# Kernel tuning notes

Measured on AMD Instinct MI355X. Metric: run time of the kernel, lower is better.

Reference implementation:

```python
import jax, jax.numpy as jnp
import numpy as np

B, N, C = 4, 8192, 512
H = 4
D = C // H  # 128
HID = 4 * C  # mlp hidden, mlp_ratio=4.0
SCALE = D ** -0.5
EPS = 1e-5


def layernorm(x, w, b):
    mu = jnp.mean(x, axis=-1, keepdims=True)
    var = jnp.var(x, axis=-1, keepdims=True)
    return (x - mu) * jax.lax.rsqrt(var + EPS) * w + b


def setup_inputs() -> dict:
    key = jax.random.key(0)
    ks = jax.random.split(key, 8)
    s = lambda fan_in: 1.0 / np.sqrt(fan_in)
    return {
        "x": jax.random.normal(ks[0], (B, N, C), jnp.float32),
        "norm1_w": jnp.ones((C,), jnp.float32),
        "norm1_b": jnp.zeros((C,), jnp.float32),
        "qkv_w": jax.random.normal(ks[1], (C, 3 * C), jnp.float32) * s(C),
        "qkv_b": jnp.zeros((3 * C,), jnp.float32),
        "lnk_w": jnp.ones((D,), jnp.float32),
        "lnk_b": jnp.zeros((D,), jnp.float32),
        "lnv_w": jnp.ones((D,), jnp.float32),
        "lnv_b": jnp.zeros((D,), jnp.float32),
        "proj_w": jax.random.normal(ks[2], (C, C), jnp.float32) * s(C),
        "proj_b": jnp.zeros((C,), jnp.float32),
        "norm2_w": jnp.ones((C,), jnp.float32),
        "norm2_b": jnp.zeros((C,), jnp.float32),
        "mlp_w1": jax.random.normal(ks[3], (C, HID), jnp.float32) * s(C),
        "mlp_b1": jnp.zeros((HID,), jnp.float32),
        "mlp_w2": jax.random.normal(ks[4], (HID, C), jnp.float32) * s(HID),
        "mlp_b2": jnp.zeros((C,), jnp.float32),
    }


def reference(x, norm1_w, norm1_b, qkv_w, qkv_b, lnk_w, lnk_b, lnv_w, lnv_b,
              proj_w, proj_b, norm2_w, norm2_b, mlp_w1, mlp_b1, mlp_w2, mlp_b2):
    shortcut = x
    xn = layernorm(x, norm1_w, norm1_b)
    qkv = xn @ qkv_w + qkv_b                       # [B,N,3C]
    qkv = qkv.reshape(B, N, 3, H, D).transpose(2, 0, 3, 1, 4)  # [3,B,H,N,D]
    q, k, v = qkv[0], qkv[1], qkv[2]
    k = layernorm(k, lnk_w, lnk_b)
    v = layernorm(v, lnv_w, lnv_b)
    context = jnp.einsum('bhnd,bhne->bhde', k, v)   # [B,H,D,D] small context
    attn = jnp.einsum('bhnd,bhde->bhne', q, context) * SCALE  # [B,H,N,D]
    attn = attn.transpose(0, 2, 1, 3).reshape(B, N, C)
    x1 = shortcut + (attn @ proj_w + proj_b)
    h = layernorm(x1, norm2_w, norm2_b)
    mlp = jax.nn.gelu(h @ mlp_w1 + mlp_b1, approximate=False) @ mlp_w2 + mlp_b2
    return x1 + mlp
```

## Files before the change

### kernel.cpp

```cpp
#include <hip/hip_runtime.h>
#include <stdint.h>


#define B_    4
#define N_    8192
#define C_    512
#define H_    4
#define D_    128
#define HID_  2048
#define M_    (B_*N_)
#define EPS_  1e-5f
#define SCALE_ 0.08838834764831845f

typedef unsigned short u16;
typedef __attribute__((ext_vector_type(8))) __bf16 bfrag_t;
typedef __attribute__((ext_vector_type(4))) float  f4_t;

__device__ __forceinline__ float bf2f(u16 a) {
    unsigned int u = ((unsigned int)a) << 16; float f;
    __builtin_memcpy(&f, &u, 4); return f;
}
__device__ __forceinline__ u16 f2bf(float f) {
    unsigned int u; __builtin_memcpy(&u, &f, 4);
    u += 0x7FFFu + ((u >> 16) & 1u);
    return (u16)(u >> 16);
}
__device__ __forceinline__ u16 f2bf_fast(float f) {
    unsigned int u; __builtin_memcpy(&u, &f, 4);
    return (u16)((u + 0x8000u) >> 16);
}

__device__ __forceinline__ float fast_gelu(float x) {
    const float kA = 2.3022084f;
    const float kB = 0.1029435f;
    float x2 = x * x;
    float e1 = __builtin_amdgcn_exp2f(x * (kB * x2 + kA));
    return x - x * __builtin_amdgcn_rcpf(e1 + 1.0f);
}

__device__ __forceinline__ void gld16(u16* lds, const u16* g) {
    void* gp = const_cast<u16*>(g);
    __builtin_amdgcn_global_load_lds((__attribute__((address_space(1))) void*)gp,
                                     (__attribute__((address_space(3))) void*)lds,
                                     16, 0, 0);
}

__global__ void wtrans(const float* __restrict__ in, u16* __restrict__ out,
                       int K, int Ncols) {
    long idx = (long)blockIdx.x * 256 + threadIdx.x;
    long total = (long)K * Ncols;
    if (idx >= total) return;
    int k = (int)(idx % K), n = (int)(idx / K);
    out[idx] = f2bf(in[(long)k * Ncols + n]);
}

__global__ __launch_bounds__(256)
void ln_rows(const float* __restrict__ in, const float* __restrict__ w,
             const float* __restrict__ b, u16* __restrict__ out) {
    long row = blockIdx.x;
    int t = threadIdx.x;
    const float* p = in + row * 512;
    float v0 = p[t], v1 = p[t + 256];
    float s = v0 + v1, q = v0 * v0 + v1 * v1;
    #pragma unroll
    for (int o = 32; o >= 1; o >>= 1) { s += __shfl_xor(s, o, 64); q += __shfl_xor(q, o, 64); }
    __shared__ float sh[8];
    int wv = t >> 6, l = t & 63;
    if (l == 0) { sh[wv] = s; sh[4 + wv] = q; }
    __syncthreads();
    s = sh[0] + sh[1] + sh[2] + sh[3];
    q = sh[4] + sh[5] + sh[6] + sh[7];
    float mu = s * (1.f / 512.f);
    float var = q * (1.f / 512.f) - mu * mu;
    float rs = rsqrtf(var + EPS_);
    out[row * 512 + t]       = f2bf((v0 - mu) * rs * w[t] + b[t]);
    out[row * 512 + t + 256] = f2bf((v1 - mu) * rs * w[t + 256] + b[t + 256]);
}

__global__ __launch_bounds__(256)
void lnkv(const u16* __restrict__ qkv,
          const float* __restrict__ kw, const float* __restrict__ kb,
          const float* __restrict__ vw, const float* __restrict__ vb,
          u16* __restrict__ kT, u16* __restrict__ vT) {
    int bh = blockIdx.x;
    int b = bh >> 2, h = bh & 3;
    int n0 = blockIdx.y * 64;
    int wv = threadIdx.x >> 6, l = threadIdx.x & 63;
    __shared__ u16 lk[128 * 68], lv[128 * 68];

    for (int r = wv; r < 64; r += 4) {
        long base = ((long)b * N_ + n0 + r) * 1536 + h * 128;
        {
            float x0 = bf2f(qkv[base + 512 + l]), x1 = bf2f(qkv[base + 512 + 64 + l]);
            float s = x0 + x1, q = x0 * x0 + x1 * x1;
            #pragma unroll
            for (int o = 32; o >= 1; o >>= 1) { s += __shfl_xor(s, o, 64); q += __shfl_xor(q, o, 64); }
            float mu = s * (1.f / 128.f), var = q * (1.f / 128.f) - mu * mu;
            float rs = rsqrtf(var + EPS_);
            lk[l * 68 + r]        = f2bf((x0 - mu) * rs * kw[l] + kb[l]);
            lk[(l + 64) * 68 + r] = f2bf((x1 - mu) * rs * kw[l + 64] + kb[l + 64]);
        }
        {
            float x0 = bf2f(qkv[base + 1024 + l]), x1 = bf2f(qkv[base + 1024 + 64 + l]);
            float s = x0 + x1, q = x0 * x0 + x1 * x1;
            #pragma unroll
            for (int o = 32; o >= 1; o >>= 1) { s += __shfl_xor(s, o, 64); q += __shfl_xor(q, o, 64); }
            float mu = s * (1.f / 128.f), var = q * (1.f / 128.f) - mu * mu;
            float rs = rsqrtf(var + EPS_);
            lv[l * 68 + r]        = f2bf((x0 - mu) * rs * vw[l] + vb[l]);
            lv[(l + 64) * 68 + r] = f2bf((x1 - mu) * rs * vw[l + 64] + vb[l + 64]);
        }
    }
    __syncthreads();
    long obase = (long)bh * D_ * N_;
    #pragma unroll 4
    for (int i = 0; i < 32; i++) {
        int idx = i * 256 + threadIdx.x;
        int d = idx >> 6, nn = idx & 63;
        kT[obase + (long)d * N_ + n0 + nn] = lk[d * 68 + nn];
        vT[obase + (long)d * N_ + n0 + nn] = lv[d * 68 + nn];
    }
}

__global__ void ctxfin(const float* __restrict__ ctxP, u16* __restrict__ ctxN) {
    int idx = blockIdx.x * 256 + threadIdx.x;
    if (idx >= 16 * 16384) return;
    int bh = idx >> 14, r = idx & 16383;
    const float* p = ctxP + (long)bh * 262144 + r;
    float s = 0.f;
    #pragma unroll
    for (int q = 0; q < 16; q++) s += p[q * 16384];
    ctxN[idx] = f2bf(s * SCALE_);
}

template<int MODE, int KTOT, int ZDIV>
__global__ __launch_bounds__(256)
void gemm_bt(const u16* __restrict__ A, int lda, int64_t aZ1, int64_t aZ2,
             const u16* __restrict__ Bt, int ldb, int64_t bZ1, int64_t bZ2,
             void* __restrict__ outv, int ldo, int64_t oZ1, int64_t oZ2,
             const float* __restrict__ bias, const float* __restrict__ resid, int ldr) {
    __shared__ __align__(16) u16 sA[128 * 32];
    __shared__ __align__(16) u16 sB[128 * 32];
    const int z = blockIdx.z;
    const int z1 = z / ZDIV, z2 = z % ZDIV;
    A  += z1 * aZ1 + z2 * aZ2;
    Bt += z1 * bZ1 + z2 * bZ2;
    const int64_t ooff = z1 * oZ1 + z2 * oZ2;
    const int m0 = blockIdx.x * 128, n0 = blockIdx.y * 128;
    const int tid = threadIdx.x, wave = tid >> 6, lane = tid & 63;
    const int wr = wave >> 1, wc = wave & 1;

    f4_t acc[4][4];
    #pragma unroll
    for (int i = 0; i < 4; i++)
        #pragma unroll
        for (int j = 0; j < 4; j++) acc[i][j] = (f4_t){0.f, 0.f, 0.f, 0.f};

    const int c0 = wave * 64 + lane, c1 = 256 + wave * 64 + lane;
    const int r0 = c0 >> 2, e0 = (c0 & 3) * 8;
    const int r1 = c1 >> 2, e1 = (c1 & 3) * 8;
    const u16* a0 = A + (int64_t)(m0 + r0) * lda + e0;
    const u16* a1 = A + (int64_t)(m0 + r1) * lda + e1;
    const u16* b0 = Bt + (int64_t)(n0 + r0) * ldb + e0;
    const u16* b1 = Bt + (int64_t)(n0 + r1) * ldb + e1;
    u16* lA0 = &sA[wave * 512];        u16* lA1 = &sA[2048 + wave * 512];
    u16* lB0 = &sB[wave * 512];        u16* lB1 = &sB[2048 + wave * 512];

    const int qd = lane >> 4, md = lane & 15;
    int aoff[4], boff[4];
    #pragma unroll
    for (int i = 0; i < 4; i++) {
        aoff[i] = (wr * 64 + i * 16 + md) * 32 + qd * 8;
        boff[i] = (wc * 64 + i * 16 + md) * 32 + qd * 8;
    }

    #pragma unroll 4
    for (int kt = 0; kt < KTOT; kt += 32) {
        __syncthreads();
        gld16(lA0, a0 + kt);  gld16(lA1, a1 + kt);
        gld16(lB0, b0 + kt);  gld16(lB1, b1 + kt);
        __syncthreads();
        bfrag_t af[4], bf[4];
        #pragma unroll
        for (int i = 0; i < 4; i++) af[i] = *(const bfrag_t*)&sA[aoff[i]];
        #pragma unroll
        for (int i = 0; i < 4; i++) bf[i] = *(const bfrag_t*)&sB[boff[i]];
        #pragma unroll
        for (int mi = 0; mi < 4; mi++)
            #pragma unroll
            for (int ni = 0; ni < 4; ni++)
                acc[mi][ni] = __builtin_amdgcn_mfma_f32_16x16x32_bf16(
                    af[mi], bf[ni], acc[mi][ni], 0, 0, 0);
    }

    #pragma unroll
    for (int mi = 0; mi < 4; mi++) {
        #pragma unroll
        for (int r = 0; r < 4; r++) {
            int m = m0 + wr * 64 + mi * 16 + qd * 4 + r;
            int64_t rowo = ooff + (int64_t)m * ldo;
            #pragma unroll
            for (int ni = 0; ni < 4; ni++) {
                int n = n0 + wc * 64 + ni * 16 + md;
                float v = acc[mi][ni][r];
                if (MODE == 0)
                    ((u16*)outv)[rowo + n] = f2bf_fast(v);
                else
                    ((float*)outv)[rowo + n] = v;
            }
        }
    }
}

#define LD_(p)      (*(const bfrag_t*)(p))
#define FENCE_      asm volatile("" ::: "memory")
#define BAR_        do { FENCE_; __builtin_amdgcn_s_barrier(); FENCE_; } while (0)
#define WVM4_       asm volatile("s_waitcnt vmcnt(4)" ::: "memory")
#define WVM0_       asm volatile("s_waitcnt vmcnt(0)" ::: "memory")
#define MFMA_(va, vb, c) c = __builtin_amdgcn_mfma_f32_16x16x32_bf16(va, vb, c, 0, 0, 0)
#define MM16_(I0) do { __builtin_amdgcn_s_setprio(1); \
  MFMA_(a0,b0,acc[(I0)+0][0]); MFMA_(a0,b1,acc[(I0)+0][1]); MFMA_(a0,b2,acc[(I0)+0][2]); MFMA_(a0,b3,acc[(I0)+0][3]); \
  MFMA_(a1,b0,acc[(I0)+1][0]); MFMA_(a1,b1,acc[(I0)+1][1]); MFMA_(a1,b2,acc[(I0)+1][2]); MFMA_(a1,b3,acc[(I0)+1][3]); \
  MFMA_(a2,b0,acc[(I0)+2][0]); MFMA_(a2,b1,acc[(I0)+2][1]); MFMA_(a2,b2,acc[(I0)+2][2]); MFMA_(a2,b3,acc[(I0)+2][3]); \
  MFMA_(a3,b0,acc[(I0)+3][0]); MFMA_(a3,b1,acc[(I0)+3][1]); MFMA_(a3,b2,acc[(I0)+3][2]); MFMA_(a3,b3,acc[(I0)+3][3]); \
  __builtin_amdgcn_s_setprio(0); } while (0)
#define STGA_(nb, kk, tt) do { \
  u16* d_ = lds + (nb) * 32768 + (kk) * 8192 + wid * 512; \
  const u16* s_ = aS + (int64_t)(tt) * 64 + (kk) * 32; \
  gld16(d_, s_); gld16(d_ + 4096, s_ + a128); } while (0)
#define STGB_(nb, kk, tt) do { \
  u16* d_ = lds + (nb) * 32768 + 16384 + (kk) * 8192 + wid * 512; \
  const u16* s_ = bS + (int64_t)(tt) * 64 + (kk) * 32; \
  gld16(d_, s_); gld16(d_ + 4096, s_ + b128); } while (0)

template<int MODE, int KTOT>
__global__ __launch_bounds__(512, 2)
void gemm256(const u16* __restrict__ A, int lda, int64_t aZ,
             const u16* __restrict__ Bt, int ldb, int64_t bZ,
             void* __restrict__ outv, int ldo, int64_t oZ,
             const float* __restrict__ bias, const float* __restrict__ resid, int ldr) {
    __shared__ __align__(16) u16 lds[65536];
    const int z = blockIdx.z;
    A += (int64_t)z * aZ;
    Bt += (int64_t)z * bZ;
    const int64_t ooff = (int64_t)z * oZ;
    const int gx = gridDim.x, gy = gridDim.y;
    const int lid = blockIdx.x + blockIdx.y * gx;
    int bx, by;
    if ((gx & 7) == 0) {
        const int j = lid >> 3;
        bx = (gx >> 3) * (lid & 7) + j / gy;
        by = j % gy;
    } else { bx = blockIdx.x; by = blockIdx.y; }
    const int m0 = bx * 256, n0 = by * 256;
    const int tid = threadIdx.x, wid = tid >> 6, lane = tid & 63;
    const int wr = wid >> 2, wc = wid & 3;
    const int md = lane & 15, qd = lane >> 4;

    f4_t acc[8][4];
    #pragma unroll
    for (int i = 0; i < 8; ++i)
        #pragma unroll
        for (int j = 0; j < 4; ++j) acc[i][j] = (f4_t){0.f, 0.f, 0.f, 0.f};

    const int srow = tid >> 2;
    const int scol = ((tid & 3) ^ ((tid >> 3) & 3)) * 8;
    const u16* aS = A  + (int64_t)(m0 + srow) * lda + scol;
    const u16* bS = Bt + (int64_t)(n0 + srow) * ldb + scol;
    const int64_t a128 = (int64_t)lda * 128, b128 = (int64_t)ldb * 128;

    const int xq = (qd ^ ((md >> 1) & 3)) * 16;
    const int aRow = (wr * 128 + md) * 64;
    const int bRow = (wc * 64 + md) * 64;
    const char* ldsc = (const char*)lds;

    constexpr int NT = KTOT / 64;

    {
        STGA_(0, 0, 0); STGB_(0, 0, 0); STGA_(0, 1, 0); STGB_(0, 1, 0);
        WVM4_; BAR_;
    }

    #pragma unroll 2
    for (int t = 0; t < NT; ++t) {
        const int cur = t & 1, nb = cur ^ 1;
        const char* cA = ldsc + cur * 65536 + aRow;
        const char* cB = ldsc + cur * 65536 + 32768 + bRow;
        const bool st = (t + 1 < NT);
        bfrag_t a0, a1, a2, a3, b0, b1, b2, b3;

        a0 = LD_(cA + xq);        a1 = LD_(cA + 1024 + xq);
        a2 = LD_(cA + 2048 + xq); a3 = LD_(cA + 3072 + xq);
        b0 = LD_(cB + xq);        b1 = LD_(cB + 1024 + xq);
        b2 = LD_(cB + 2048 + xq); b3 = LD_(cB + 3072 + xq);
        if (st) STGA_(nb, 0, t + 1);
        BAR_;
        MM16_(0);

        a0 = LD_(cA + 4096 + xq); a1 = LD_(cA + 5120 + xq);
        a2 = LD_(cA + 6144 + xq); a3 = LD_(cA + 7168 + xq);
        if (st) STGB_(nb, 0, t + 1);
        BAR_;
        MM16_(4);

        if (st) { WVM4_; } else { WVM0_; }
        BAR_;

        a0 = LD_(cA + 16384 + xq);        a1 = LD_(cA + 17408 + xq);
        a2 = LD_(cA + 18432 + xq);        a3 = LD_(cA + 19456 + xq);
        b0 = LD_(cB + 16384 + xq);        b1 = LD_(cB + 17408 + xq);
        b2 = LD_(cB + 18432 + xq);        b3 = LD_(cB + 19456 + xq);
        if (st) STGA_(nb, 1, t + 1);
        BAR_;
        MM16_(0);

        a0 = LD_(cA + 20480 + xq); a1 = LD_(cA + 21504 + xq);
        a2 = LD_(cA + 22528 + xq); a3 = LD_(cA + 23552 + xq);
        if (st) STGB_(nb, 1, t + 1);
        BAR_;
        MM16_(4);

        if (st) { WVM4_; } else { WVM0_; }
        BAR_;
    }

    #pragma unroll
    for (int i = 0; i < 8; ++i) {
        #pragma unroll
        for (int rr = 0; rr < 4; ++rr) {
            const int m = m0 + wr * 128 + i * 16 + qd * 4 + rr;
            const int64_t rowo = ooff + (int64_t)m * ldo;
            #pragma unroll
            for (int j = 0; j < 4; ++j) {
                const int n = n0 + wc * 64 + j * 16 + md;
                float v = acc[i][j][rr];
                if (MODE == 1 || MODE == 2 || MODE == 3) v += bias[n];
                if (MODE == 2) v = fast_gelu(v);
                if (MODE == 3) v += resid[ooff + (int64_t)m * ldr + n];
                if (MODE == 3)
                    ((float*)outv)[rowo + n] = v;
                else
                    ((u16*)outv)[rowo + n] = f2bf_fast(v);
            }
        }
    }
}

#undef LD_
#undef FENCE_
#undef BAR_
#undef WVM4_
#undef WVM0_
#undef MFMA_
#undef MM16_
#undef STGA_
#undef STGB_

extern "C" void kernel_launch(void* const* d_in, const int* in_sizes, int n_in,
                              void* d_out, int out_size, void* d_ws, size_t ws_size,
                              hipStream_t stream) {
    const float* x      = (const float*)d_in[0];
    const float* n1w    = (const float*)d_in[1];
    const float* n1b    = (const float*)d_in[2];
    const float* qkv_w  = (const float*)d_in[3];
    const float* qkv_b  = (const float*)d_in[4];
    const float* lnk_w  = (const float*)d_in[5];
    const float* lnk_b  = (const float*)d_in[6];
    const float* lnv_w  = (const float*)d_in[7];
    const float* lnv_b  = (const float*)d_in[8];
    const float* proj_w = (const float*)d_in[9];
    const float* proj_b = (const float*)d_in[10];
    const float* n2w    = (const float*)d_in[11];
    const float* n2b    = (const float*)d_in[12];
    const float* w1     = (const float*)d_in[13];
    const float* b1     = (const float*)d_in[14];
    const float* w2     = (const float*)d_in[15];
    const float* b2     = (const float*)d_in[16];
    float* out = (float*)d_out;

    char* ws = (char*)d_ws;
    u16*  qkvWT = (u16*)(ws + 0);
    u16*  projT = (u16*)(ws + 1572864);
    u16*  w1T   = (u16*)(ws + 2097152);
    u16*  w2T   = (u16*)(ws + 4194304);
    u16*  ctxN  = (u16*)(ws + 7340032);
    u16*  bufA  = (u16*)(ws + 7864320);
    u16*  qkv   = (u16*)(ws + 41418752);
    u16*  hid   = (u16*)(ws + 41418752);
    u16*  kT    = (u16*)(ws + 142082048);
    u16*  vT    = (u16*)(ws + 175636480);
    float* ctxP = (float*)(ws + 7864320);
    u16*  wqT   = (u16*)(ws + 7864320 + 16777216);

    dim3 blk(256);
    dim3 blk5(512);

    wtrans<<<dim3(512 * 1536 / 256), blk, 0, stream>>>(qkv_w, qkvWT, 512, 1536);
    wtrans<<<dim3(512 * 512 / 256),  blk, 0, stream>>>(proj_w, projT, 512, 512);
    wtrans<<<dim3(512 * 2048 / 256), blk, 0, stream>>>(w1, w1T, 512, 2048);
    wtrans<<<dim3(2048 * 512 / 256), blk, 0, stream>>>(w2, w2T, 2048, 512);

    ln_rows<<<dim3(M_), blk, 0, stream>>>(x, n1w, n1b, bufA);

    gemm256<1, 512><<<dim3(M_ / 256, 1536 / 256, 1), blk5, 0, stream>>>(
        bufA, 512, 0, qkvWT, 512, 0, (void*)qkv, 1536, 0, qkv_b, nullptr, 0);

    lnkv<<<dim3(B_ * H_, N_ / 64), blk, 0, stream>>>(qkv, lnk_w, lnk_b, lnv_w, lnv_b, kT, vT);

    gemm_bt<5, 512, 16><<<dim3(1, 1, B_ * H_ * 16), blk, 0, stream>>>(
        kT, N_, (int64_t)D_ * N_, 512,  vT, N_, (int64_t)D_ * N_, 512,
        (void*)ctxP, 128, 262144, 16384,  nullptr, nullptr, 0);
    ctxfin<<<dim3(16 * 16384 / 256), blk, 0, stream>>>(ctxP, ctxN);

    gemm_bt<0, 128, 4><<<dim3(4, 1, 16), blk, 0, stream>>>(
        projT, 512, 0, 128,  ctxN, 128, 65536, 16384,
        (void*)wqT, 512, 262144, 128,  nullptr, nullptr, 0);

    gemm256<3, 512><<<dim3(N_ / 256, 512 / 256, B_), blk5, 0, stream>>>(
        qkv, 1536, (int64_t)N_ * 1536,  wqT, 512, 262144,
        (void*)out, 512, (int64_t)N_ * 512,  proj_b, x, 512);

    ln_rows<<<dim3(M_), blk, 0, stream>>>(out, n2w, n2b, bufA);

    gemm256<2, 512><<<dim3(M_ / 256, HID_ / 256, 1), blk5, 0, stream>>>(
        bufA, 512, 0, w1T, 512, 0, (void*)hid, HID_, 0, b1, nullptr, 0);

    gemm256<3, 2048><<<dim3(M_ / 256, 512 / 256, 1), blk5, 0, stream>>>(
        hid, HID_, 0, w2T, HID_, 0, (void*)out, 512, 0, b2, out, 512);
}
```

Before: 574.7 us.

## Swap MFMA operands for vectorized GEMM epilogue and tile weight transpose via LDS

The 256x256 GEMM swaps the A and B operands of each MFMA so that every lane's accumulator holds four consecutive output columns. The epilogue can then load bias and residual as float4 and write packed bf16x4 or float4 stores instead of scalar ones. The weight-transpose kernel becomes a 64x64 LDS-tiled transpose so its global reads and writes are coalesced. This removes scattered scalar stores in the memory-heavy epilogues, at the cost of depending on the changed accumulator lane layout being mapped correctly.

```diff
diff --git a/kernel.cpp b/kernel.cpp
--- a/kernel.cpp
+++ b/kernel.cpp
@@ -13,20 +13,22 @@
 #define SCALE_ 0.08838834764831845f
 
 typedef unsigned short u16;
+typedef unsigned int u32;
 typedef __attribute__((ext_vector_type(8))) __bf16 bfrag_t;
 typedef __attribute__((ext_vector_type(4))) float  f4_t;
+typedef __attribute__((ext_vector_type(2))) u32    u32x2;
 
 __device__ __forceinline__ float bf2f(u16 a) {
-    unsigned int u = ((unsigned int)a) << 16; float f;
+    u32 u = ((u32)a) << 16; float f;
     __builtin_memcpy(&f, &u, 4); return f;
 }
 __device__ __forceinline__ u16 f2bf(float f) {
-    unsigned int u; __builtin_memcpy(&u, &f, 4);
+    u32 u; __builtin_memcpy(&u, &f, 4);
     u += 0x7FFFu + ((u >> 16) & 1u);
     return (u16)(u >> 16);
 }
 __device__ __forceinline__ u16 f2bf_fast(float f) {
-    unsigned int u; __builtin_memcpy(&u, &f, 4);
+    u32 u; __builtin_memcpy(&u, &f, 4);
     return (u16)((u + 0x8000u) >> 16);
 }
 
@@ -45,13 +47,24 @@
                                      16, 0, 0);
 }
 
-__global__ void wtrans(const float* __restrict__ in, u16* __restrict__ out,
-                       int K, int Ncols) {
-    long idx = (long)blockIdx.x * 256 + threadIdx.x;
-    long total = (long)K * Ncols;
-    if (idx >= total) return;
-    int k = (int)(idx % K), n = (int)(idx / K);
-    out[idx] = f2bf(in[(long)k * Ncols + n]);
+__global__ __launch_bounds__(256)
+void wtrans(const float* __restrict__ in, u16* __restrict__ out,
+            int K, int Ncols) {
+    const int nb = Ncols >> 6;
+    const int k0 = (blockIdx.x / nb) << 6, n0 = (blockIdx.x % nb) << 6;
+    __shared__ u16 tile[64][65];
+    const int tx = threadIdx.x & 63, ty = threadIdx.x >> 6;
+    #pragma unroll
+    for (int r = 0; r < 16; ++r) {
+        int k = ty + r * 4;
+        tile[k][tx] = f2bf(in[(long)(k0 + k) * Ncols + n0 + tx]);
+    }
+    __syncthreads();
+    #pragma unroll
+    for (int r = 0; r < 16; ++r) {
+        int n = ty + r * 4;
+        out[(long)(n0 + n) * K + k0 + tx] = tile[tx][n];
+    }
 }
 
 __global__ __launch_bounds__(256)
@@ -219,10 +232,10 @@
 #define WVM0_       asm volatile("s_waitcnt vmcnt(0)" ::: "memory")
 #define MFMA_(va, vb, c) c = __builtin_amdgcn_mfma_f32_16x16x32_bf16(va, vb, c, 0, 0, 0)
 #define MM16_(I0) do { __builtin_amdgcn_s_setprio(1); \
-  MFMA_(a0,b0,acc[(I0)+0][0]); MFMA_(a0,b1,acc[(I0)+0][1]); MFMA_(a0,b2,acc[(I0)+0][2]); MFMA_(a0,b3,acc[(I0)+0][3]); \
-  MFMA_(a1,b0,acc[(I0)+1][0]); MFMA_(a1,b1,acc[(I0)+1][1]); MFMA_(a1,b2,acc[(I0)+1][2]); MFMA_(a1,b3,acc[(I0)+1][3]); \
-  MFMA_(a2,b0,acc[(I0)+2][0]); MFMA_(a2,b1,acc[(I0)+2][1]); MFMA_(a2,b2,acc[(I0)+2][2]); MFMA_(a2,b3,acc[(I0)+2][3]); \
-  MFMA_(a3,b0,acc[(I0)+3][0]); MFMA_(a3,b1,acc[(I0)+3][1]); MFMA_(a3,b2,acc[(I0)+3][2]); MFMA_(a3,b3,acc[(I0)+3][3]); \
+  MFMA_(b0,a0,acc[(I0)+0][0]); MFMA_(b1,a0,acc[(I0)+0][1]); MFMA_(b2,a0,acc[(I0)+0][2]); MFMA_(b3,a0,acc[(I0)+0][3]); \
+  MFMA_(b0,a1,acc[(I0)+1][0]); MFMA_(b1,a1,acc[(I0)+1][1]); MFMA_(b2,a1,acc[(I0)+1][2]); MFMA_(b3,a1,acc[(I0)+1][3]); \
+  MFMA_(b0,a2,acc[(I0)+2][0]); MFMA_(b1,a2,acc[(I0)+2][1]); MFMA_(b2,a2,acc[(I0)+2][2]); MFMA_(b3,a2,acc[(I0)+2][3]); \
+  MFMA_(b0,a3,acc[(I0)+3][0]); MFMA_(b1,a3,acc[(I0)+3][1]); MFMA_(b2,a3,acc[(I0)+3][2]); MFMA_(b3,a3,acc[(I0)+3][3]); \
   __builtin_amdgcn_s_setprio(0); } while (0)
 #define STGA_(nb, kk, tt) do { \
   u16* d_ = lds + (nb) * 32768 + (kk) * 8192 + wid * 512; \
@@ -326,21 +339,29 @@
 
     #pragma unroll
     for (int i = 0; i < 8; ++i) {
-        #pragma unroll
-        for (int rr = 0; rr < 4; ++rr) {
-            const int m = m0 + wr * 128 + i * 16 + qd * 4 + rr;
-            const int64_t rowo = ooff + (int64_t)m * ldo;
-            #pragma unroll
-            for (int j = 0; j < 4; ++j) {
-                const int n = n0 + wc * 64 + j * 16 + md;
-                float v = acc[i][j][rr];
-                if (MODE == 1 || MODE == 2 || MODE == 3) v += bias[n];
-                if (MODE == 2) v = fast_gelu(v);
-                if (MODE == 3) v += resid[ooff + (int64_t)m * ldr + n];
-                if (MODE == 3)
-                    ((float*)outv)[rowo + n] = v;
-                else
-                    ((u16*)outv)[rowo + n] = f2bf_fast(v);
+        const int m = m0 + wr * 128 + i * 16 + md;
+        const int64_t rowo = ooff + (int64_t)m * ldo;
+        #pragma unroll
+        for (int j = 0; j < 4; ++j) {
+            const int n = n0 + wc * 64 + j * 16 + qd * 4;
+            f4_t v = acc[i][j];
+            if (MODE == 1 || MODE == 2 || MODE == 3) {
+                const f4_t bq = *(const f4_t*)&bias[n];
+                v.x += bq.x; v.y += bq.y; v.z += bq.z; v.w += bq.w;
+            }
+            if (MODE == 2) {
+                v.x = fast_gelu(v.x); v.y = fast_gelu(v.y);
+                v.z = fast_gelu(v.z); v.w = fast_gelu(v.w);
+            }
+            if (MODE == 3) {
+                const f4_t r4 = *(const f4_t*)&resid[ooff + (int64_t)m * ldr + n];
+                v.x += r4.x; v.y += r4.y; v.z += r4.z; v.w += r4.w;
+                *(f4_t*)&((float*)outv)[rowo + n] = v;
+            } else {
+                u32x2 pk;
+                pk.x = (u32)f2bf_fast(v.x) | ((u32)f2bf_fast(v.y) << 16);
+                pk.y = (u32)f2bf_fast(v.z) | ((u32)f2bf_fast(v.w) << 16);
+                *(u32x2*)&((u16*)outv)[rowo + n] = pk;
             }
         }
     }
@@ -395,10 +416,10 @@
     dim3 blk(256);
     dim3 blk5(512);
 
-    wtrans<<<dim3(512 * 1536 / 256), blk, 0, stream>>>(qkv_w, qkvWT, 512, 1536);
-    wtrans<<<dim3(512 * 512 / 256),  blk, 0, stream>>>(proj_w, projT, 512, 512);
-    wtrans<<<dim3(512 * 2048 / 256), blk, 0, stream>>>(w1, w1T, 512, 2048);
-    wtrans<<<dim3(2048 * 512 / 256), blk, 0, stream>>>(w2, w2T, 2048, 512);
+    wtrans<<<dim3((512 / 64) * (1536 / 64)), blk, 0, stream>>>(qkv_w, qkvWT, 512, 1536);
+    wtrans<<<dim3((512 / 64) * (512 / 64)),  blk, 0, stream>>>(proj_w, projT, 512, 512);
+    wtrans<<<dim3((512 / 64) * (2048 / 64)), blk, 0, stream>>>(w1, w1T, 512, 2048);
+    wtrans<<<dim3((2048 / 64) * (512 / 64)), blk, 0, stream>>>(w2, w2T, 2048, 512);
 
     ln_rows<<<dim3(M_), blk, 0, stream>>>(x, n1w, n1b, bufA);
 
```

Result: faster. 549.7 us (-4.3%).
